# Performance work log

Hardware: AMD Instinct MI355X
Metric: run time of the kernel (lower is better)

## Reference

```python
import jax, jax.numpy as jnp
import numpy as np
from jax import lax

B, N, D = 4, 4096, 1024
H, DH, K = 8, 128, 256  # heads, dim_head, linformer k
KERNEL = 32
PAD = (15, 16)  # torch padding='same' for even kernel: left=(k-1)//2, right=rest


def setup_inputs() -> dict:
    key = jax.random.key(0)
    ks = jax.random.split(key, 7)
    s = 0.02
    return {
        "x": jax.random.normal(ks[0], (B, N, D), dtype=jnp.float32),
        "Wq": jax.random.normal(ks[1], (D, D), dtype=jnp.float32) * s,
        "Wk": jax.random.normal(ks[2], (D, D), dtype=jnp.float32) * s,
        "Wpk": jax.random.normal(ks[3], (K, N, KERNEL), dtype=jnp.float32) * s,
        "bpk": jax.random.normal(ks[4], (K,), dtype=jnp.float32) * s,
        "Wo": jax.random.normal(ks[5], (D, D), dtype=jnp.float32) * s,
        "bo": jax.random.normal(ks[6], (D,), dtype=jnp.float32) * s,
    }


def reference(x, Wq, Wk, Wpk, bpk, Wo, bo):
    b, n, d = x.shape
    # linear projections (torch Linear: y = x @ W.T)
    q = x @ Wq.T                       # (b, n, h*dh)
    keys = x @ Wk.T                    # (b, n, h*dh)
    # Conv1d over feature length with seq positions as channels: (b, n, d) -> (b, k, d)
    keys = lax.conv_general_dilated(
        keys, Wpk, window_strides=(1,), padding=[PAD],
        dimension_numbers=("NCH", "OIH", "NCH"),
    ) + bpk[None, :, None]             # (b, K, h*dh)
    values = keys                      # share_kv=True
    # split heads
    q = q.reshape(b, n, H, DH).transpose(0, 2, 1, 3)        # (b, h, n, dh)
    kk = keys.reshape(b, K, H, DH).transpose(0, 2, 1, 3)    # (b, h, K, dh)
    vv = values.reshape(b, K, H, DH).transpose(0, 2, 1, 3)  # (b, h, K, dh)
    dots = jnp.einsum("bhnd,bhkd->bhnk", q, kk) * (DH ** -0.5)
    attn = jax.nn.softmax(dots, axis=-1)                    # dropout p=0.0 (eval)
    out = jnp.einsum("bhnk,bhkd->bhnd", attn, vv)
    out = out.transpose(0, 2, 1, 3).reshape(b, n, H * DH)
    return out @ Wo.T + bo
```

## Files before the change

### kernel.cpp

```cpp
#include <hip/hip_runtime.h>


typedef short v8s __attribute__((ext_vector_type(8)));
typedef float v4f __attribute__((ext_vector_type(4)));

#define MFMA16(a, b, c) __builtin_amdgcn_mfma_f32_16x16x32_bf16((a), (b), (c), 0, 0, 0)
#define WAITV(N) asm volatile("s_waitcnt vmcnt(" #N ")" ::: "memory")
#define SBAR() __builtin_amdgcn_s_barrier()

__device__ __forceinline__ unsigned short f2bf(float f) {
  unsigned int u = __float_as_uint(f);
  u += 0x7fffu + ((u >> 16) & 1u);
  return (unsigned short)(u >> 16);
}

__device__ __forceinline__ v8s cvt8(float4 a, float4 b) {
  v8s v;
  v[0] = (short)f2bf(a.x); v[1] = (short)f2bf(a.y);
  v[2] = (short)f2bf(a.z); v[3] = (short)f2bf(a.w);
  v[4] = (short)f2bf(b.x); v[5] = (short)f2bf(b.y);
  v[6] = (short)f2bf(b.z); v[7] = (short)f2bf(b.w);
  return v;
}

__device__ __forceinline__ void gld16(void* lds, const void* g) {
  __builtin_amdgcn_global_load_lds(
      (const __attribute__((address_space(1))) void*)g,
      (__attribute__((address_space(3))) void*)lds, 16, 0, 0);
}

__device__ __forceinline__ const v8s* frag_ptr(const short* base, int row, int g) {
  return (const v8s*)(base + row * 32 + (((g ^ (row >> 1)) & 3) << 3));
}

__global__ __launch_bounds__(256) void k_cvt(const float* __restrict__ src,
                                             short* __restrict__ dst, int n8) {
  const int i = blockIdx.x * 256 + threadIdx.x;
  if (i >= n8) return;
  const float4* s = (const float4*)src;
  ((v8s*)dst)[i] = cvt8(s[2 * i], s[2 * i + 1]);
}

__global__ __launch_bounds__(256) void k_reorder_wpk(const float* __restrict__ Wpk,
                                                     short* __restrict__ Wr) {
  __shared__ short T[64][40];
  const int k  = blockIdx.x >> 6;
  const int n0 = (blockIdx.x & 63) << 6;
  const int tid = threadIdx.x;
  {
    const int i = tid >> 2, t0 = (tid & 3) << 3;
    const float* p = Wpk + ((size_t)k * 4096 + n0 + i) * 32 + t0;
    float4 a = *(const float4*)p, b = *(const float4*)(p + 4);
    *(v8s*)&T[i][t0] = cvt8(a, b);
  }
  __syncthreads();
  {
    const int t = tid >> 3, j0 = (tid & 7) << 3;
    v8s o;
#pragma unroll
    for (int q = 0; q < 8; ++q) o[q] = T[j0 + q][t];
    *(v8s*)(Wr + ((size_t)t * 256 + k) * 4096 + n0 + j0) = o;
  }
}

__global__ __launch_bounds__(256) void k_zero_pad(short* __restrict__ KpTp) {
  const int idx = blockIdx.x * 256 + threadIdx.x;
  const int ridx = idx >> 9, col8 = idx & 511;
  const int b = ridx >> 5, rr = ridx & 31;
  const int row = (rr < 15) ? rr : 1039 + (rr - 15);
  v8s z = {0, 0, 0, 0, 0, 0, 0, 0};
  *(v8s*)(KpTp + ((size_t)b * 1056 + row) * 4096 + col8 * 8) = z;
}

__global__ __launch_bounds__(256) void k_gemm_qk_v3(const short* __restrict__ xbf,
                                                    const short* __restrict__ Wqk,
                                                    short* __restrict__ Qbf,
                                                    short* __restrict__ Kp) {
  __shared__ short As[2][128][32];
  __shared__ short Bs[2][128][32];
  const int tid = threadIdx.x, lane = tid & 63, w = tid >> 6;
  const int m0 = blockIdx.x * 128, j0 = blockIdx.y * 128;
  const int wr = (w >> 1) * 64, wc = (w & 1) * 64;
  const int l15 = lane & 15, g = lane >> 4;
  const int sr = lane >> 2, sseg = lane & 3;

  v4f acc[4][4];
#pragma unroll
  for (int i = 0; i < 4; ++i)
#pragma unroll
    for (int j = 0; j < 4; ++j) acc[i][j] = (v4f)0.0f;

  auto stage = [&](int buf, int k0) {
#pragma unroll
    for (int q0 = 0; q0 < 2; ++q0) {
      const int rblk = (w * 2 + q0) << 4, r = rblk + sr;
      const int co = ((sseg ^ (r >> 1)) & 3) << 3;
      gld16(&As[buf][rblk][0], xbf + (size_t)(m0 + r) * 1024 + k0 + co);
      gld16(&Bs[buf][rblk][0], Wqk + (size_t)(j0 + r) * 1024 + k0 + co);
    }
  };

  stage(0, 0);
#pragma unroll 1
  for (int p = 0, buf = 0; p < 32; ++p, buf ^= 1) {
    if (p + 1 < 32) stage(buf ^ 1, (p + 1) * 32);
    if (p < 31) { WAITV(4); } else { WAITV(0); }
    SBAR();
    v8s af[4], bf4[4];
#pragma unroll
    for (int mi = 0; mi < 4; ++mi)
      af[mi] = *frag_ptr(&As[buf][0][0], wr + mi * 16 + l15, g);
#pragma unroll
    for (int ni = 0; ni < 4; ++ni)
      bf4[ni] = *frag_ptr(&Bs[buf][0][0], wc + ni * 16 + l15, g);
#pragma unroll
    for (int ni = 0; ni < 4; ++ni)
#pragma unroll
      for (int mi = 0; mi < 4; ++mi)
        acc[mi][ni] = MFMA16(af[mi], bf4[ni], acc[mi][ni]);
    SBAR();
  }
  const int rbase = (lane >> 4) * 4;
#pragma unroll
  for (int mi = 0; mi < 4; ++mi)
#pragma unroll
    for (int ni = 0; ni < 4; ++ni) {
      const int col = j0 + wc + ni * 16 + l15;
      short* dst = (col < 1024) ? Qbf : Kp;
      const int cj = (col < 1024) ? col : col - 1024;
#pragma unroll
      for (int r = 0; r < 4; ++r) {
        const int row = m0 + wr + mi * 16 + rbase + r;
        dst[(size_t)row * 1024 + cj] = (short)f2bf(acc[mi][ni][r]);
      }
    }
}

__global__ __launch_bounds__(256) void k_transpose_pad(const short* __restrict__ src,
                                                       short* __restrict__ dst) {
  __shared__ short T[64][72];
  const int r0 = blockIdx.x * 64, c0 = blockIdx.y * 64, b = blockIdx.z;
  const int tid = threadIdx.x;
  {
    const int i = tid >> 2, q = (tid & 3) << 4;
    const short* ps = src + ((size_t)b * 4096 + r0 + i) * 1024 + c0 + q;
    *(v8s*)&T[i][q]     = *(const v8s*)ps;
    *(v8s*)&T[i][q + 8] = *(const v8s*)(ps + 8);
  }
  __syncthreads();
  {
    const int j = tid >> 2, p = (tid & 3) << 4;
    v8s o0, o1;
#pragma unroll
    for (int t = 0; t < 8; ++t) o0[t] = T[p + t][j];
#pragma unroll
    for (int t = 0; t < 8; ++t) o1[t] = T[p + 8 + t][j];
    short* pd = dst + ((size_t)b * 1056 + 15 + c0 + j) * 4096 + r0 + p;
    *(v8s*)pd = o0;
    *(v8s*)(pd + 8) = o1;
  }
}

__global__ __launch_bounds__(512, 2) void k_conv_v4(const short* __restrict__ Wr,
                                                    const short* __restrict__ KpTp,
                                                    float* __restrict__ Pq) {
  __shared__ short A[3][256][32];
  __shared__ short Kt[2][384][32];
  const int bid = blockIdx.x;
  const int ns = (bid & 7) | (((bid >> 7) & 1) << 3);
  const int j  = (bid >> 3) & 15;
  const int b = j >> 2, nt = j & 3;
  const int D0 = nt * 256;
  const int nbase = ns * 256;
  const int tid = threadIdx.x, lane = tid & 63, w = tid >> 6;
  const int wm = (w >> 2) * 128, wn = (w & 3) * 64;
  const int l15 = lane & 15, g = lane >> 4;
  const int lr = lane >> 2, lseg = lane & 3;
  const short* KpTb = KpTp + (size_t)b * 1056 * 4096;

  v4f acc[8][4];
#pragma unroll
  for (int mi = 0; mi < 8; ++mi)
#pragma unroll
    for (int ni = 0; ni < 4; ++ni) acc[mi][ni] = (v4f)0.0f;

  auto stageA = [&](int buf, int s2, int q) {
    const int t2 = s2 & 31, c2 = s2 >> 5;
    const int rblk = q * 128 + w * 16;
    const int row = rblk + lr;
    const int sg = ((lseg ^ (row >> 1)) & 3) << 3;
    gld16(&A[buf][rblk][0],
          Wr + ((size_t)t2 * 256 + row) * 4096 + nbase + c2 * 32 + sg);
  };
  auto stageKt = [&](int buf, int c1, int q) {
    const int rblk = q * 128 + w * 16;
    const int row = rblk + lr;
    const int srow = row < 287 ? row : 286;
    const int sg = ((lseg ^ (row >> 1)) & 3) << 3;
    gld16(&Kt[buf][rblk][0],
          KpTb + (size_t)(D0 + srow) * 4096 + nbase + c1 * 32 + sg);
  };

  stageA(0, 0, 0); stageA(0, 0, 1);
  stageKt(0, 0, 0); stageKt(0, 0, 1); stageKt(0, 0, 2);
  stageA(1, 1, 0); stageA(1, 1, 1);
  WAITV(2);
  SBAR();

  int ab = 0, pab = 2;
#pragma unroll 1
  for (int s = 0; s < 256; ++s) {
    const int t = s & 31, c = s >> 5;
    const short* Abp = &A[ab][0][0];
    const short* Ktp = &Kt[c & 1][0][0];
    v8s bq[4], aq[4];
#pragma unroll
    for (int ni = 0; ni < 4; ++ni)
      bq[ni] = *frag_ptr(Ktp, wn + ni * 16 + l15 + t, g);
#pragma unroll
    for (int mi = 0; mi < 4; ++mi)
      aq[mi] = *frag_ptr(Abp, wm + mi * 16 + l15, g);
    if (s + 2 < 256) stageA(pab, s + 2, 0);
    SBAR();
    __builtin_amdgcn_s_setprio(1);
#pragma unroll
    for (int ni = 0; ni < 4; ++ni)
#pragma unroll
      for (int mi = 0; mi < 4; ++mi)
        acc[mi][ni] = MFMA16(aq[mi], bq[ni], acc[mi][ni]);
    __builtin_amdgcn_s_setprio(0);
    SBAR();
    v8s aq2[4];
#pragma unroll
    for (int mi = 0; mi < 4; ++mi)
      aq2[mi] = *frag_ptr(Abp, wm + 64 + mi * 16 + l15, g);
    const bool ktst = ((unsigned)(t - 24) <= 2u) && (c < 7);
    if (s + 2 < 256) stageA(pab, s + 2, 1);
    if (ktst) stageKt((c + 1) & 1, c + 1, t - 24);
    SBAR();
    __builtin_amdgcn_s_setprio(1);
#pragma unroll
    for (int ni = 0; ni < 4; ++ni)
#pragma unroll
      for (int mi = 0; mi < 4; ++mi)
        acc[4 + mi][ni] = MFMA16(aq2[mi], bq[ni], acc[4 + mi][ni]);
    __builtin_amdgcn_s_setprio(0);
    if (s < 254) {
      if (ktst) { WAITV(3); } else { WAITV(2); }
    } else if (s == 254) {
      WAITV(0);
    }
    SBAR();
    pab = ab; ab = (ab == 2) ? 0 : ab + 1;
  }

  float* Pp = Pq + (size_t)(ns * 4 + b) * 262144;
#pragma unroll
  for (int mi = 0; mi < 8; ++mi)
#pragma unroll
    for (int ni = 0; ni < 4; ++ni) {
      const int col = D0 + wn + ni * 16 + l15;
#pragma unroll
      for (int r = 0; r < 4; ++r)
        Pp[(size_t)(wm + mi * 16 + g * 4 + r) * 1024 + col] = acc[mi][ni][r];
    }
}

__global__ __launch_bounds__(256) void k_reduce_kc(const float* __restrict__ P,
                                                   const float* __restrict__ bpk,
                                                   float* __restrict__ Kc) {
  const int i = (blockIdx.x * 256 + threadIdx.x) * 4;
  const float bias = bpk[(i >> 10) & 255];
  float4 s; s.x = bias; s.y = bias; s.z = bias; s.w = bias;
#pragma unroll
  for (int ns = 0; ns < 16; ++ns) {
    float4 v = *(const float4*)(P + (size_t)ns * 1048576 + i);
    s.x += v.x; s.y += v.y; s.z += v.z; s.w += v.w;
  }
  *(float4*)(Kc + i) = s;
}

__global__ __launch_bounds__(256) void k_kc_post(const float* __restrict__ Kc,
                                                 short* __restrict__ Kcbf,
                                                 short* __restrict__ KcT) {
  __shared__ short T[64][72];
  const int k0 = blockIdx.x * 64, d0 = blockIdx.y * 64, b = blockIdx.z;
  const int tid = threadIdx.x;
  {
    const int i = tid >> 2, q = (tid & 3) << 4;
    const float* ps = Kc + (size_t)(b * 256 + k0 + i) * 1024 + d0 + q;
    float4 f0 = *(const float4*)ps,       f1 = *(const float4*)(ps + 4);
    float4 f2 = *(const float4*)(ps + 8), f3 = *(const float4*)(ps + 12);
    v8s v0 = cvt8(f0, f1), v1 = cvt8(f2, f3);
    *(v8s*)&T[i][q] = v0;
    *(v8s*)&T[i][q + 8] = v1;
    short* pc = Kcbf + (size_t)(b * 256 + k0 + i) * 1024 + d0 + q;
    *(v8s*)pc = v0;
    *(v8s*)(pc + 8) = v1;
  }
  __syncthreads();
  {
    const int j = tid >> 2, p = (tid & 3) << 4;
    v8s o0, o1;
#pragma unroll
    for (int t = 0; t < 8; ++t) o0[t] = T[p + t][j];
#pragma unroll
    for (int t = 0; t < 8; ++t) o1[t] = T[p + 8 + t][j];
    short* pd = KcT + (size_t)(b * 1024 + d0 + j) * 256 + k0 + p;
    *(v8s*)pd = o0;
    *(v8s*)(pd + 8) = o1;
  }
}

__global__ __launch_bounds__(256) void k_attn(const short* __restrict__ Qbf,
                                              const short* __restrict__ Kcbf,
                                              const short* __restrict__ KcT,
                                              short* __restrict__ AO) {
  __shared__ short P[4][16][264];
  const int nt = blockIdx.x, h = blockIdx.y, b = blockIdx.z;
  const int tid = threadIdx.x, lane = tid & 63, w = tid >> 6;
  const int l15 = lane & 15, lg4 = (lane >> 4) * 4, lg8 = (lane >> 4) * 8;
  const float scale = 0.08838834764831845f;
  const size_t qb  = (size_t)b * 4096 * 1024 + (size_t)h * 128;
  const size_t kb  = (size_t)b * 256 * 1024 + (size_t)h * 128;
  const size_t vtb = ((size_t)b * 1024 + (size_t)h * 128) * 256;
  short (*Pw)[264] = P[w];
  const int n_wave = nt * 128 + w * 32;

#pragma unroll 1
  for (int half = 0; half < 2; ++half) {
    const int nbase = n_wave + half * 16;
    v8s aq[4];
#pragma unroll
    for (int kt = 0; kt < 4; ++kt)
      aq[kt] = *(const v8s*)(Qbf + qb + (size_t)(nbase + l15) * 1024 + kt * 32 + lg8);

    v4f dacc[16];
#pragma unroll
    for (int ct = 0; ct < 16; ++ct) dacc[ct] = (v4f)0.0f;
#pragma unroll 1
    for (int kt = 0; kt < 4; ++kt) {
#pragma unroll
      for (int ct = 0; ct < 16; ++ct) {
        v8s bk = *(const v8s*)(Kcbf + kb + (size_t)(ct * 16 + l15) * 1024 + kt * 32 + lg8);
        dacc[ct] = MFMA16(aq[kt], bk, dacc[ct]);
      }
    }
#pragma unroll
    for (int ct = 0; ct < 16; ++ct) dacc[ct] = dacc[ct] * scale;
    v4f m4 = dacc[0];
#pragma unroll
    for (int ct = 1; ct < 16; ++ct)
#pragma unroll
      for (int r = 0; r < 4; ++r) m4[r] = fmaxf(m4[r], dacc[ct][r]);
#pragma unroll
    for (int off = 1; off < 16; off <<= 1)
#pragma unroll
      for (int r = 0; r < 4; ++r) m4[r] = fmaxf(m4[r], __shfl_xor(m4[r], off, 64));
    v4f ssum = (v4f)0.0f;
#pragma unroll
    for (int ct = 0; ct < 16; ++ct)
#pragma unroll
      for (int r = 0; r < 4; ++r) {
        const float e = __expf(dacc[ct][r] - m4[r]);
        ssum[r] += e;
        Pw[lg4 + r][ct * 16 + l15] = (short)f2bf(e);
      }
#pragma unroll
    for (int off = 1; off < 16; off <<= 1)
#pragma unroll
      for (int r = 0; r < 4; ++r) ssum[r] += __shfl_xor(ssum[r], off, 64);
    __syncthreads();

    v4f oacc[8];
#pragma unroll
    for (int ct = 0; ct < 8; ++ct) oacc[ct] = (v4f)0.0f;
#pragma unroll 1
    for (int kt2 = 0; kt2 < 8; ++kt2) {
      v8s pa = *(const v8s*)&Pw[l15][kt2 * 32 + lg8];
#pragma unroll
      for (int ct = 0; ct < 8; ++ct) {
        v8s bv = *(const v8s*)(KcT + vtb + (size_t)(ct * 16 + l15) * 256 + kt2 * 32 + lg8);
        oacc[ct] = MFMA16(pa, bv, oacc[ct]);
      }
    }
    v4f inv;
#pragma unroll
    for (int r = 0; r < 4; ++r) inv[r] = 1.0f / ssum[r];
#pragma unroll
    for (int ct = 0; ct < 8; ++ct)
#pragma unroll
      for (int r = 0; r < 4; ++r)
        AO[qb + (size_t)(nbase + lg4 + r) * 1024 + ct * 16 + l15] =
            (short)f2bf(oacc[ct][r] * inv[r]);
    __syncthreads();
  }
}

__global__ __launch_bounds__(256) void k_gemm_out_v3(const short* __restrict__ AO,
                                                     const short* __restrict__ Wobf,
                                                     const float* __restrict__ bo,
                                                     float* __restrict__ out) {
  __shared__ short As[2][128][32];
  __shared__ short Bs[2][128][32];
  const int tid = threadIdx.x, lane = tid & 63, w = tid >> 6;
  const int m0 = blockIdx.x * 128, j0 = blockIdx.y * 128;
  const int wr = (w >> 1) * 64, wc = (w & 1) * 64;
  const int l15 = lane & 15, g = lane >> 4;
  const int sr = lane >> 2, sseg = lane & 3;

  v4f acc[4][4];
#pragma unroll
  for (int i = 0; i < 4; ++i)
#pragma unroll
    for (int j = 0; j < 4; ++j) acc[i][j] = (v4f)0.0f;

  auto stage = [&](int buf, int k0) {
#pragma unroll
    for (int q0 = 0; q0 < 2; ++q0) {
      const int rblk = (w * 2 + q0) << 4, r = rblk + sr;
      const int co = ((sseg ^ (r >> 1)) & 3) << 3;
      gld16(&As[buf][rblk][0], AO + (size_t)(m0 + r) * 1024 + k0 + co);
      gld16(&Bs[buf][rblk][0], Wobf + (size_t)(j0 + r) * 1024 + k0 + co);
    }
  };

  stage(0, 0);
#pragma unroll 1
  for (int p = 0, buf = 0; p < 32; ++p, buf ^= 1) {
    if (p + 1 < 32) stage(buf ^ 1, (p + 1) * 32);
    if (p < 31) { WAITV(4); } else { WAITV(0); }
    SBAR();
    v8s af[4], bf4[4];
#pragma unroll
    for (int mi = 0; mi < 4; ++mi)
      af[mi] = *frag_ptr(&As[buf][0][0], wr + mi * 16 + l15, g);
#pragma unroll
    for (int ni = 0; ni < 4; ++ni)
      bf4[ni] = *frag_ptr(&Bs[buf][0][0], wc + ni * 16 + l15, g);
#pragma unroll
    for (int ni = 0; ni < 4; ++ni)
#pragma unroll
      for (int mi = 0; mi < 4; ++mi)
        acc[mi][ni] = MFMA16(af[mi], bf4[ni], acc[mi][ni]);
    SBAR();
  }
  const int rbase = (lane >> 4) * 4;
#pragma unroll
  for (int mi = 0; mi < 4; ++mi)
#pragma unroll
    for (int ni = 0; ni < 4; ++ni) {
      const int col = j0 + wc + ni * 16 + l15;
      const float bias = bo[col];
#pragma unroll
      for (int r = 0; r < 4; ++r) {
        const int row = m0 + wr + mi * 16 + rbase + r;
        out[(size_t)row * 1024 + col] = acc[mi][ni][r] + bias;
      }
    }
}

extern "C" void kernel_launch(void* const* d_in, const int* in_sizes, int n_in,
                              void* d_out, int out_size, void* d_ws, size_t ws_size,
                              hipStream_t stream) {
  const float* x   = (const float*)d_in[0];
  const float* Wq  = (const float*)d_in[1];
  const float* Wk  = (const float*)d_in[2];
  const float* Wpk = (const float*)d_in[3];
  const float* bpk = (const float*)d_in[4];
  const float* Wo  = (const float*)d_in[5];
  const float* bo  = (const float*)d_in[6];

  const size_t OFF_WR   = 0;
  const size_t OFF_XBF  = 67108864;
  const size_t OFF_WQK  = 100663296;
  const size_t OFF_KPTP = 67108864;
  const size_t OFF_KCBF = 67108864;
  const size_t OFF_KCT  = 69206016;
  const size_t OFF_WOBF = 101711872;
  const size_t OFF_QBF  = 104857600;
  const size_t OFF_KP   = 138412032;
  const size_t OFF_KC   = 171966464;
  const size_t NEED     = 176160768;
  if (ws_size < NEED) return;

  char* ws = (char*)d_ws;
  short* Wr   = (short*)(ws + OFF_WR);
  short* xbf  = (short*)(ws + OFF_XBF);
  short* Wqk  = (short*)(ws + OFF_WQK);
  short* KpTp = (short*)(ws + OFF_KPTP);
  short* Kcbf = (short*)(ws + OFF_KCBF);
  short* KcT  = (short*)(ws + OFF_KCT);
  short* Wobf = (short*)(ws + OFF_WOBF);
  short* Qbf  = (short*)(ws + OFF_QBF);
  short* Kp   = (short*)(ws + OFF_KP);
  float* Kc   = (float*)(ws + OFF_KC);
  short* AO   = Kp;
  float* Ppart = (float*)d_out;
  float* outp = (float*)d_out;

  k_cvt<<<dim3(8192), dim3(256), 0, stream>>>(x, xbf, 16777216 / 8);
  k_cvt<<<dim3(512),  dim3(256), 0, stream>>>(Wq, Wqk, 1048576 / 8);
  k_cvt<<<dim3(512),  dim3(256), 0, stream>>>(Wk, Wqk + 1048576, 1048576 / 8);
  k_reorder_wpk<<<dim3(16384), dim3(256), 0, stream>>>(Wpk, Wr);
  k_gemm_qk_v3<<<dim3(128, 16), dim3(256), 0, stream>>>(xbf, Wqk, Qbf, Kp);
  k_transpose_pad<<<dim3(64, 16, 4), dim3(256), 0, stream>>>(Kp, KpTp);
  k_cvt<<<dim3(512), dim3(256), 0, stream>>>(Wo, Wobf, 1048576 / 8);
  k_zero_pad<<<dim3(256), dim3(256), 0, stream>>>(KpTp);
  k_conv_v4<<<dim3(256), dim3(512), 0, stream>>>(Wr, KpTp, Ppart);
  k_reduce_kc<<<dim3(1024), dim3(256), 0, stream>>>(Ppart, bpk, Kc);
  k_kc_post<<<dim3(4, 16, 4), dim3(256), 0, stream>>>(Kc, Kcbf, KcT);
  k_attn<<<dim3(32, 8, 4), dim3(256), 0, stream>>>(Qbf, Kcbf, KcT, AO);
  k_gemm_out_v3<<<dim3(128, 8), dim3(256), 0, stream>>>(AO, Wobf, bo, outp);
}
```

Measured before the change: 633.1 us.

## Halve conv output tile width and double grid for more resident blocks

Shrinks the conv kernel's per-block output tile from 256 to 128 feature columns, cuts each wave's accumulator to 4x4 MFMA tiles, and launches 512 blocks instead of 256. It also merges the two half-step MFMA phases into one with a single barrier per step, and raises launch bounds to allow more blocks per CU. The aim is better occupancy, fewer barriers and lower register and LDS use. The cost is that each A (Wr) tile now feeds fewer output columns, so Wr global traffic doubles and reuse per load drops.

```diff
diff --git a/kernel.cpp b/kernel.cpp
--- a/kernel.cpp
+++ b/kernel.cpp
@@ -161,26 +161,26 @@
   }
 }
 
-__global__ __launch_bounds__(512, 2) void k_conv_v4(const short* __restrict__ Wr,
+__global__ __launch_bounds__(512, 4) void k_conv_v5(const short* __restrict__ Wr,
                                                     const short* __restrict__ KpTp,
                                                     float* __restrict__ Pq) {
   __shared__ short A[3][256][32];
-  __shared__ short Kt[2][384][32];
+  __shared__ short Kt[2][160][32];
   const int bid = blockIdx.x;
-  const int ns = (bid & 7) | (((bid >> 7) & 1) << 3);
-  const int j  = (bid >> 3) & 15;
-  const int b = j >> 2, nt = j & 3;
-  const int D0 = nt * 256;
+  const int ns = (bid & 7) | (((bid >> 8) & 1) << 3);
+  const int j  = (bid >> 3) & 31;
+  const int b = j >> 3, nt = j & 7;
+  const int D0 = nt * 128;
   const int nbase = ns * 256;
   const int tid = threadIdx.x, lane = tid & 63, w = tid >> 6;
-  const int wm = (w >> 2) * 128, wn = (w & 3) * 64;
+  const int wm = (w >> 1) * 64, wn = (w & 1) * 64;
   const int l15 = lane & 15, g = lane >> 4;
   const int lr = lane >> 2, lseg = lane & 3;
   const short* KpTb = KpTp + (size_t)b * 1056 * 4096;
 
-  v4f acc[8][4];
-#pragma unroll
-  for (int mi = 0; mi < 8; ++mi)
+  v4f acc[4][4];
+#pragma unroll
+  for (int mi = 0; mi < 4; ++mi)
 #pragma unroll
     for (int ni = 0; ni < 4; ++ni) acc[mi][ni] = (v4f)0.0f;
 
@@ -195,14 +195,15 @@
   auto stageKt = [&](int buf, int c1, int q) {
     const int rblk = q * 128 + w * 16;
     const int row = rblk + lr;
-    const int srow = row < 287 ? row : 286;
+    const int srow = row < 159 ? row : 158;
     const int sg = ((lseg ^ (row >> 1)) & 3) << 3;
     gld16(&Kt[buf][rblk][0],
           KpTb + (size_t)(D0 + srow) * 4096 + nbase + c1 * 32 + sg);
   };
 
   stageA(0, 0, 0); stageA(0, 0, 1);
-  stageKt(0, 0, 0); stageKt(0, 0, 1); stageKt(0, 0, 2);
+  stageKt(0, 0, 0);
+  if (w < 2) stageKt(0, 0, 1);
   stageA(1, 1, 0); stageA(1, 1, 1);
   WAITV(2);
   SBAR();
@@ -213,15 +214,18 @@
     const int t = s & 31, c = s >> 5;
     const short* Abp = &A[ab][0][0];
     const short* Ktp = &Kt[c & 1][0][0];
-    v8s bq[4], aq[4];
+    v8s aq[4], bq[4];
+#pragma unroll
+    for (int mi = 0; mi < 4; ++mi)
+      aq[mi] = *frag_ptr(Abp, wm + mi * 16 + l15, g);
 #pragma unroll
     for (int ni = 0; ni < 4; ++ni)
       bq[ni] = *frag_ptr(Ktp, wn + ni * 16 + l15 + t, g);
-#pragma unroll
-    for (int mi = 0; mi < 4; ++mi)
-      aq[mi] = *frag_ptr(Abp, wm + mi * 16 + l15, g);
-    if (s + 2 < 256) stageA(pab, s + 2, 0);
-    SBAR();
+    if (s + 2 < 256) { stageA(pab, s + 2, 0); stageA(pab, s + 2, 1); }
+    const bool kt0 = (t == 26) && (c < 7);
+    const bool kt1 = (t == 27) && (c < 7);
+    if (kt0) stageKt((c + 1) & 1, c + 1, 0);
+    if (kt1 && w < 2) stageKt((c + 1) & 1, c + 1, 1);
     __builtin_amdgcn_s_setprio(1);
 #pragma unroll
     for (int ni = 0; ni < 4; ++ni)
@@ -229,24 +233,8 @@
       for (int mi = 0; mi < 4; ++mi)
         acc[mi][ni] = MFMA16(aq[mi], bq[ni], acc[mi][ni]);
     __builtin_amdgcn_s_setprio(0);
-    SBAR();
-    v8s aq2[4];
-#pragma unroll
-    for (int mi = 0; mi < 4; ++mi)
-      aq2[mi] = *frag_ptr(Abp, wm + 64 + mi * 16 + l15, g);
-    const bool ktst = ((unsigned)(t - 24) <= 2u) && (c < 7);
-    if (s + 2 < 256) stageA(pab, s + 2, 1);
-    if (ktst) stageKt((c + 1) & 1, c + 1, t - 24);
-    SBAR();
-    __builtin_amdgcn_s_setprio(1);
-#pragma unroll
-    for (int ni = 0; ni < 4; ++ni)
-#pragma unroll
-      for (int mi = 0; mi < 4; ++mi)
-        acc[4 + mi][ni] = MFMA16(aq2[mi], bq[ni], acc[4 + mi][ni]);
-    __builtin_amdgcn_s_setprio(0);
     if (s < 254) {
-      if (ktst) { WAITV(3); } else { WAITV(2); }
+      if (kt0 || kt1) { WAITV(3); } else { WAITV(2); }
     } else if (s == 254) {
       WAITV(0);
     }
@@ -256,7 +244,7 @@
 
   float* Pp = Pq + (size_t)(ns * 4 + b) * 262144;
 #pragma unroll
-  for (int mi = 0; mi < 8; ++mi)
+  for (int mi = 0; mi < 4; ++mi)
 #pragma unroll
     for (int ni = 0; ni < 4; ++ni) {
       const int col = D0 + wn + ni * 16 + l15;
@@ -507,7 +495,7 @@
   k_transpose_pad<<<dim3(64, 16, 4), dim3(256), 0, stream>>>(Kp, KpTp);
   k_cvt<<<dim3(512), dim3(256), 0, stream>>>(Wo, Wobf, 1048576 / 8);
   k_zero_pad<<<dim3(256), dim3(256), 0, stream>>>(KpTp);
-  k_conv_v4<<<dim3(256), dim3(512), 0, stream>>>(Wr, KpTp, Ppart);
+  k_conv_v5<<<dim3(512), dim3(512), 0, stream>>>(Wr, KpTp, Ppart);
   k_reduce_kc<<<dim3(1024), dim3(256), 0, stream>>>(Ppart, bpk, Kc);
   k_kc_post<<<dim3(4, 16, 4), dim3(256), 0, stream>>>(Kc, Kcbf, KcT);
   k_attn<<<dim3(32, 8, 4), dim3(256), 0, stream>>>(Qbf, Kcbf, KcT, AO);
```

After: 608.3 us. -3.9%, faster.
